# Kernel optimization log

Measured on AMD Instinct MI355X. Metric: run time of the kernel, lower is better.

The kernel has to match this reference:

```python
import jax, jax.numpy as jnp
import numpy as np

B, T = 128, 64          # batch, episode length
OB, AC, L, H = 32, 8, 128, 256  # ob_dim, ac_dim, latent_dim, mlp hidden
N_SUB = 4               # fixed Dopri5 substeps per interval (replaces adaptive PID controller)


def setup_inputs() -> dict:
    key = jax.random.key(0)
    ks = jax.random.split(key, 12)
    g = lambda k, shape, fan: jax.random.normal(k, shape, jnp.float32) / np.sqrt(fan)
    return {
        "ob": jax.random.normal(ks[0], (B, OB), jnp.float32),
        "acs": jax.random.normal(ks[1], (B, T, AC), jnp.float32),
        # strictly increasing timestamps (cumsum of uniform increments)
        "times": jnp.cumsum(jax.random.uniform(ks[2], (B, T), jnp.float32, 0.02, 0.1), axis=1),
        # ob encoder MLP (OB -> H -> L), relu hidden, identity out
        "We0": g(ks[3], (H, OB), OB), "be0": jnp.zeros((H,), jnp.float32),
        "We1": g(ks[4], (L, H), H), "be1": jnp.zeros((L,), jnp.float32),
        # latent dynamics MLP (L -> H -> H -> L)
        "Wd0": g(ks[5], (H, L), L), "bd0": jnp.zeros((H,), jnp.float32),
        "Wd1": g(ks[6], (H, H), H), "bd1": jnp.zeros((H,), jnp.float32),
        "Wd2": g(ks[7], (L, H), H), "bd2": jnp.zeros((L,), jnp.float32),
        # ob decoder MLP (L -> H -> OB)
        "Wo0": g(ks[8], (H, L), L), "bo0": jnp.zeros((H,), jnp.float32),
        "Wo1": g(ks[9], (OB, H), H), "bo1": jnp.zeros((OB,), jnp.float32),
        # GRU cell (input=AC, hidden=L), equinox layout: gates [r, z, n]
        "Wih": g(ks[10], (3 * L, AC), AC), "Whh": g(ks[11], (3 * L, L), L),
        "bih": jnp.zeros((3 * L,), jnp.float32), "bn": jnp.zeros((L,), jnp.float32),
    }


def reference(ob, acs, times, We0, be0, We1, be1, Wd0, bd0, Wd1, bd1, Wd2, bd2,
              Wo0, bo0, Wo1, bo1, Wih, Whh, bih, bn):
    def f(y):  # dynamics MLP on batched latent (B, L) -> (B, L)
        h1 = jax.nn.relu(y @ Wd0.T + bd0)
        h2 = jax.nn.relu(h1 @ Wd1.T + bd1)
        return h2 @ Wd2.T + bd2

    def gru(x, h):  # equinox GRUCell math, batched
        ir, iz, inn = jnp.split(x @ Wih.T + bih, 3, axis=-1)
        hr, hz, hn = jnp.split(h @ Whh.T, 3, axis=-1)
        r = jax.nn.sigmoid(ir + hr)
        z = jax.nn.sigmoid(iz + hz)
        n = jnp.tanh(inn + r * (hn + bn))
        return (1.0 - z) * n + z * h

    def dopri5_step(y, h):  # one Dopri5 (RK45) step, h: (B, 1) per-sample step size
        k1 = f(y)
        k2 = f(y + h * (0.2 * k1))
        k3 = f(y + h * (3/40 * k1 + 9/40 * k2))
        k4 = f(y + h * (44/45 * k1 - 56/15 * k2 + 32/9 * k3))
        k5 = f(y + h * (19372/6561 * k1 - 25360/2187 * k2 + 64448/6561 * k3 - 212/729 * k4))
        k6 = f(y + h * (9017/3168 * k1 - 355/33 * k2 + 46732/5247 * k3 + 49/176 * k4 - 5103/18656 * k5))
        return y + h * (35/384 * k1 + 500/1113 * k3 + 125/192 * k4 - 2187/6784 * k5 + 11/84 * k6)

    def integrate(y, dt):  # integrate latent ODE from 0 to dt with N_SUB fixed Dopri5 steps
        h = (dt / N_SUB)[:, None]
        return jax.lax.fori_loop(0, N_SUB, lambda i, yy: dopri5_step(yy, h), y)

    # encode first observation, consume first action
    latent0 = jax.nn.relu(ob @ We0.T + be0) @ We1.T + be1  # (B, L)
    latent0 = gru(acs[:, 0], latent0)

    dts = jnp.diff(times, axis=1)  # (B, T-1)

    def step(latent, xs):
        ac, dt = xs
        latent = integrate(latent, dt)
        latent = gru(ac, latent)
        return latent, latent

    xs = (jnp.swapaxes(acs[:, 1:], 0, 1), dts.T)  # time-major for scan
    _, lat_seq = jax.lax.scan(step, latent0, xs)  # (T-1, B, L)

    latents = jnp.concatenate([latent0[None], lat_seq], axis=0)  # (T, B, L)
    latents = jnp.swapaxes(latents, 0, 1)  # (B, T, L)

    h1 = jax.nn.relu(latents @ Wo0.T + bo0)
    return h1 @ Wo1.T + bo1  # (B, T, OB)
```

## Files before the change

kernel.cpp:

```cpp
#include <hip/hip_runtime.h>
#include <stdint.h>

#define NBATCH 128
#define NT     64
#define OBD    32
#define ACD    8
#define LDIM   128
#define HDIM   256

typedef _Float16 h2 __attribute__((ext_vector_type(2)));
typedef float    f4 __attribute__((ext_vector_type(4)));

#if defined(__has_builtin)
#  if __has_builtin(__builtin_amdgcn_fdot2)
#    define HAVE_FDOT2 1
#  endif
#endif

__device__ __forceinline__ float dot2f(h2 a, h2 b, float c) {
#ifdef HAVE_FDOT2
  return __builtin_amdgcn_fdot2(a, b, c, false);
#else
  return c + (float)a[0] * (float)b[0] + (float)a[1] * (float)b[1];
#endif
}

__device__ __forceinline__ h2 pkh(float a, float b) {
  h2 r; r[0] = (_Float16)a; r[1] = (_Float16)b; return r;
}

__device__ __forceinline__ h2 bch(float x) { return __builtin_bit_cast(h2, x); }

__device__ __forceinline__ float sigmf(float x) { return 1.0f / (1.0f + expf(-x)); }

#define DOT4(W, I, Q) \
    a0 = dot2f(W[4*(I)+0], bch(Q.x), a0); \
    a1 = dot2f(W[4*(I)+1], bch(Q.y), a1); \
    a2 = dot2f(W[4*(I)+2], bch(Q.z), a2); \
    a3 = dot2f(W[4*(I)+3], bch(Q.w), a3);

__global__ __launch_bounds__(512, 1)
void ode_rnn_kernel(const float* __restrict__ ob,   const float* __restrict__ acs,
                    const float* __restrict__ times,
                    const float* __restrict__ We0,  const float* __restrict__ be0,
                    const float* __restrict__ We1,  const float* __restrict__ be1,
                    const float* __restrict__ Wd0,  const float* __restrict__ bd0,
                    const float* __restrict__ Wd1,  const float* __restrict__ bd1,
                    const float* __restrict__ Wd2,  const float* __restrict__ bd2,
                    const float* __restrict__ Wo0,  const float* __restrict__ bo0,
                    const float* __restrict__ Wo1,  const float* __restrict__ bo1,
                    const float* __restrict__ Wih,  const float* __restrict__ Whh,
                    const float* __restrict__ bih,  const float* __restrict__ bn,
                    float* __restrict__ out)
{
  const int t    = threadIdx.x;
  const int b    = blockIdx.x;
  const int p    = t >> 1;
  const int sub  = t & 1;
  const int r3   = t >> 2;
  const int ksub = t & 3;

  __shared__ __align__(16) float s_lat[LDIM];
  __shared__ __align__(16) float s_k[5][LDIM];
  __shared__ __align__(16) float s_gz[LDIM];
  __shared__ __align__(16) float s_gin[LDIM];
  __shared__ __align__(16) float s_ghn[LDIM];
  __shared__ __align__(16) float s_tmp[HDIM];
  __shared__ __align__(16) float s_obs[OBD];
  __shared__ __align__(16) float s_times[NT];
  __shared__ __align__(16) float s_acs[NT * ACD];
  __shared__ __align__(16) h2    s_in16[LDIM / 2];
  __shared__ __align__(16) h2    s_a16[HDIM / 2];
  __shared__ __align__(16) h2    s_b16[HDIM / 2 + 24];

  h2 w0[32], w1[64], w2[32], q0[32], q1[8];
  {
    const float2* pp = (const float2*)(Wd0 + p * LDIM + sub * 64);
#pragma unroll
    for (int i = 0; i < 32; ++i) { float2 v = pp[i]; w0[i] = pkh(v.x, v.y); }
  }
  {
    const float2* pp = (const float2*)(Wd1 + p * HDIM + sub * 128);
#pragma unroll
    for (int i = 0; i < 64; ++i) { float2 v = pp[i]; w1[i] = pkh(v.x, v.y); }
  }
  {
    const float2* pp = (const float2*)(Wd2 + r3 * HDIM + ksub * 64);
#pragma unroll
    for (int i = 0; i < 32; ++i) { float2 v = pp[i]; w2[i] = pkh(v.x, v.y); }
  }
  {
    const float2* pp = (const float2*)(Wo0 + p * LDIM + sub * 64);
#pragma unroll
    for (int i = 0; i < 32; ++i) { float2 v = pp[i]; q0[i] = pkh(v.x, v.y); }
  }
  {
    const float2* pp = (const float2*)(Wo1 + (t >> 4) * HDIM + (t & 15) * 16);
#pragma unroll
    for (int i = 0; i < 8; ++i) { float2 v = pp[i]; q1[i] = pkh(v.x, v.y); }
  }
  float wi[8];
  if (t < 3 * LDIM) {
#pragma unroll
    for (int j = 0; j < ACD; ++j) wi[j] = Wih[t * ACD + j];
  } else {
#pragma unroll
    for (int j = 0; j < ACD; ++j) wi[j] = 0.0f;
  }

  const float bb0 = bd0[p];
  const float bb1 = bd1[p];
  const float bb2 = bd2[r3];
  const float rb0 = bo0[p];
  const float rb1 = bo1[t >> 4];
  const float gbA = (t < 3 * LDIM) ? bih[t] : 0.0f;
  const float bnr = (t < LDIM) ? bn[t] : 0.0f;

  auto substep = [&](float hs) {
#pragma unroll
    for (int s = 0; s < 6; ++s) {
      float a0, a1, a2, a3, v;
      a0 = a1 = a2 = a3 = 0.0f;
      {
        const f4* src = ((const f4*)s_in16) + sub * 8;
#pragma unroll
        for (int i = 0; i < 8; ++i) { f4 q = src[i]; DOT4(w0, i, q) }
      }
      v = a0 + a1 + a2 + a3;
      v += __shfl_xor(v, 1);
      v = fmaxf(v + bb0, 0.0f);
      { float ov = __shfl_xor(v, 2); if ((t & 3) == 0) s_a16[t >> 2] = pkh(v, ov); }
      __syncthreads();
      a0 = a1 = a2 = a3 = 0.0f;
      {
        const f4* src = ((const f4*)s_a16) + sub * 16;
#pragma unroll
        for (int i = 0; i < 16; ++i) { f4 q = src[i]; DOT4(w1, i, q) }
      }
      v = a0 + a1 + a2 + a3;
      v += __shfl_xor(v, 1);
      v = fmaxf(v + bb1, 0.0f);
      { float ov = __shfl_xor(v, 2);
        if ((t & 3) == 0) s_b16[(t >> 2) + ((t >> 7) << 3)] = pkh(v, ov); }
      __syncthreads();
      a0 = a1 = a2 = a3 = 0.0f;
      {
        const f4* src = ((const f4*)s_b16) + ksub * 10;
#pragma unroll
        for (int i = 0; i < 8; ++i) { f4 q = src[i]; DOT4(w2, i, q) }
      }
      v = a0 + a1 + a2 + a3;
      v += __shfl_xor(v, 1);
      v += __shfl_xor(v, 2);
      float kv = v + bb2;
      if (s < 5 && (t & 3) == 0) s_k[s][r3] = kv;
      float base = s_lat[r3];
      float z;
      if (s == 0)
        z = base + hs * (0.2f * kv);
      else if (s == 1)
        z = base + hs * ((3.0f/40.0f)*s_k[0][r3] + (9.0f/40.0f)*kv);
      else if (s == 2)
        z = base + hs * ((44.0f/45.0f)*s_k[0][r3] - (56.0f/15.0f)*s_k[1][r3]
                       + (32.0f/9.0f)*kv);
      else if (s == 3)
        z = base + hs * ((19372.0f/6561.0f)*s_k[0][r3] - (25360.0f/2187.0f)*s_k[1][r3]
                       + (64448.0f/6561.0f)*s_k[2][r3] - (212.0f/729.0f)*kv);
      else if (s == 4)
        z = base + hs * ((9017.0f/3168.0f)*s_k[0][r3] - (355.0f/33.0f)*s_k[1][r3]
                       + (46732.0f/5247.0f)*s_k[2][r3] + (49.0f/176.0f)*s_k[3][r3]
                       - (5103.0f/18656.0f)*kv);
      else
        z = base + hs * ((35.0f/384.0f)*s_k[0][r3] + (500.0f/1113.0f)*s_k[2][r3]
                       + (125.0f/192.0f)*s_k[3][r3] - (2187.0f/6784.0f)*s_k[4][r3]
                       + (11.0f/84.0f)*kv);
      { float ov = __shfl_xor(z, 4); if ((t & 7) == 0) s_in16[t >> 3] = pkh(z, ov); }
      if (s == 5 && (t & 3) == 0) s_lat[r3] = z;
      __syncthreads();
    }
  };

  auto gru = [&](int ts) {
    __syncthreads();
    float ig = gbA, hg = 0.0f;
    if (t < 3 * LDIM) {
      const float* xa = s_acs + ts * ACD;
#pragma unroll
      for (int j = 0; j < ACD; ++j) ig += wi[j] * xa[j];
      const f4* wh = (const f4*)(Whh + t * LDIM);
      const f4* xl = (const f4*)s_lat;
#pragma unroll
      for (int k2 = 0; k2 < LDIM / 4; ++k2) {
        f4 w = wh[k2], x = xl[k2];
        hg += w.x*x.x + w.y*x.y + w.z*x.z + w.w*x.w;
      }
    }
    if (t >= LDIM && t < 2 * LDIM)          s_gz[t - LDIM] = ig + hg;
    else if (t >= 2 * LDIM && t < 3 * LDIM) { s_gin[t - 2*LDIM] = ig; s_ghn[t - 2*LDIM] = hg; }
    __syncthreads();
    if (t < LDIM) {
      float rg = sigmf(ig + hg);
      float zg = sigmf(s_gz[t]);
      float ng = tanhf(s_gin[t] + rg * (s_ghn[t] + bnr));
      float y  = (1.0f - zg) * ng + zg * s_lat[t];
      s_lat[t] = y;
      float ov = __shfl_xor(y, 1);
      if (!(t & 1)) s_in16[t >> 1] = pkh(y, ov);
    }
  };

  auto decode = [&](int ts) {
    __syncthreads();
    float a0 = 0, a1 = 0, a2 = 0, a3 = 0, v;
    {
      const f4* src = ((const f4*)s_in16) + sub * 8;
#pragma unroll
      for (int i = 0; i < 8; ++i) { f4 q = src[i]; DOT4(q0, i, q) }
    }
    v = a0 + a1 + a2 + a3;
    v += __shfl_xor(v, 1);
    v = fmaxf(v + rb0, 0.0f);
    { float ov = __shfl_xor(v, 2); if ((t & 3) == 0) s_a16[t >> 2] = pkh(v, ov); }
    __syncthreads();
    a0 = a1 = a2 = a3 = 0;
    {
      const f4* src = ((const f4*)s_a16) + (t & 15) * 2;
#pragma unroll
      for (int i = 0; i < 2; ++i) {
        f4 q = src[i];
        a0 = dot2f(q1[4*i+0], bch(q.x), a0);
        a1 = dot2f(q1[4*i+1], bch(q.y), a1);
        a2 = dot2f(q1[4*i+2], bch(q.z), a2);
        a3 = dot2f(q1[4*i+3], bch(q.w), a3);
      }
    }
    v = a0 + a1 + a2 + a3;
    v += __shfl_xor(v, 1);
    v += __shfl_xor(v, 2);
    v += __shfl_xor(v, 4);
    v += __shfl_xor(v, 8);
    if ((t & 15) == 0) out[((size_t)b * NT + ts) * OBD + (t >> 4)] = v + rb1;
    __syncthreads();
  };

  if (t < OBD) s_obs[t] = ob[b * OBD + t];
  if (t < NT)  s_times[t] = times[b * NT + t];
  s_acs[t] = acs[(size_t)b * NT * ACD + t];
  __syncthreads();
  if (t < HDIM) {
    float acc = be0[t];
    const float* wr = We0 + t * OBD;
#pragma unroll
    for (int j = 0; j < OBD; ++j) acc += wr[j] * s_obs[j];
    s_tmp[t] = fmaxf(acc, 0.0f);
  }
  __syncthreads();
  {
    const f4* wr = (const f4*)(We1 + r3 * HDIM + ksub * 64);
    const f4* xs = (const f4*)(s_tmp + ksub * 64);
    float acc = 0.0f;
#pragma unroll
    for (int k = 0; k < 16; ++k) {
      f4 w = wr[k], x = xs[k];
      acc += w.x*x.x + w.y*x.y + w.z*x.z + w.w*x.w;
    }
    acc += __shfl_xor(acc, 1);
    acc += __shfl_xor(acc, 2);
    if ((t & 3) == 0) s_lat[r3] = acc + be1[r3];
  }

  gru(0);
  decode(0);

#pragma unroll 1
  for (int ts = 1; ts < NT; ++ts) {
    float hs = 0.25f * (s_times[ts] - s_times[ts - 1]);
#pragma unroll 1
    for (int su = 0; su < 4; ++su) substep(hs);
    gru(ts);
    decode(ts);
  }
}

extern "C" void kernel_launch(void* const* d_in, const int* in_sizes, int n_in,
                              void* d_out, int out_size, void* d_ws, size_t ws_size,
                              hipStream_t stream) {
  (void)in_sizes; (void)n_in; (void)d_ws; (void)ws_size; (void)out_size;
  const float* ob    = (const float*)d_in[0];
  const float* acs   = (const float*)d_in[1];
  const float* times = (const float*)d_in[2];
  const float* We0   = (const float*)d_in[3];
  const float* be0   = (const float*)d_in[4];
  const float* We1   = (const float*)d_in[5];
  const float* be1   = (const float*)d_in[6];
  const float* Wd0   = (const float*)d_in[7];
  const float* bd0   = (const float*)d_in[8];
  const float* Wd1   = (const float*)d_in[9];
  const float* bd1   = (const float*)d_in[10];
  const float* Wd2   = (const float*)d_in[11];
  const float* bd2   = (const float*)d_in[12];
  const float* Wo0   = (const float*)d_in[13];
  const float* bo0   = (const float*)d_in[14];
  const float* Wo1   = (const float*)d_in[15];
  const float* bo1   = (const float*)d_in[16];
  const float* Wih   = (const float*)d_in[17];
  const float* Whh   = (const float*)d_in[18];
  const float* bih   = (const float*)d_in[19];
  const float* bn    = (const float*)d_in[20];

  ode_rnn_kernel<<<dim3(NBATCH), dim3(512), 0, stream>>>(
      ob, acs, times, We0, be0, We1, be1, Wd0, bd0, Wd1, bd1, Wd2, bd2,
      Wo0, bo0, Wo1, bo1, Wih, Whh, bih, bn, (float*)d_out);
}
```

Before: 2.461 ms.

## Double threads per block to 1024 and split dot products finer

Grows the block from 512 to 1024 threads, so every matvec in the Dopri5 substep, GRU and decoder is split across twice as many lanes. Each lane holds half as many register-resident fp16 weights, and partial sums are combined with extra shuffle stages. Shared-memory activation buffers get padded layouts to reduce bank conflicts. The decoder's first layer now reads Wo0 from global memory each timestep instead of keeping it in registers. Per-lane serial work on the latency-bound recurrence goes down, at the cost of more shuffles, heavier barriers across 16 waves, and extra global weight reads in the decoder.

```diff
diff --git a/kernel.cpp b/kernel.cpp
--- a/kernel.cpp
+++ b/kernel.cpp
@@ -39,7 +39,7 @@
     a2 = dot2f(W[4*(I)+2], bch(Q.z), a2); \
     a3 = dot2f(W[4*(I)+3], bch(Q.w), a3);
 
-__global__ __launch_bounds__(512, 1)
+__global__ __launch_bounds__(1024)
 void ode_rnn_kernel(const float* __restrict__ ob,   const float* __restrict__ acs,
                     const float* __restrict__ times,
                     const float* __restrict__ We0,  const float* __restrict__ be0,
@@ -53,15 +53,20 @@
                     const float* __restrict__ bih,  const float* __restrict__ bn,
                     float* __restrict__ out)
 {
-  const int t    = threadIdx.x;
-  const int b    = blockIdx.x;
-  const int p    = t >> 1;
-  const int sub  = t & 1;
-  const int r3   = t >> 2;
-  const int ksub = t & 3;
+  const int t  = threadIdx.x;
+  const int b  = blockIdx.x;
+  const int p  = t >> 2;
+  const int qs = t & 3;
+  const int r  = t >> 3;
+  const int es = t & 7;
+  const int o  = t >> 5;
+  const int s5 = t & 31;
+  const int gr = t >> 1;
+  const int kh = t & 1;
 
   __shared__ __align__(16) float s_lat[LDIM];
   __shared__ __align__(16) float s_k[5][LDIM];
+  __shared__ __align__(16) float s_gr[LDIM];
   __shared__ __align__(16) float s_gz[LDIM];
   __shared__ __align__(16) float s_gin[LDIM];
   __shared__ __align__(16) float s_ghn[LDIM];
@@ -69,51 +74,50 @@
   __shared__ __align__(16) float s_obs[OBD];
   __shared__ __align__(16) float s_times[NT];
   __shared__ __align__(16) float s_acs[NT * ACD];
-  __shared__ __align__(16) h2    s_in16[LDIM / 2];
-  __shared__ __align__(16) h2    s_a16[HDIM / 2];
-  __shared__ __align__(16) h2    s_b16[HDIM / 2 + 24];
-
-  h2 w0[32], w1[64], w2[32], q0[32], q1[8];
-  {
-    const float2* pp = (const float2*)(Wd0 + p * LDIM + sub * 64);
-#pragma unroll
-    for (int i = 0; i < 32; ++i) { float2 v = pp[i]; w0[i] = pkh(v.x, v.y); }
-  }
-  {
-    const float2* pp = (const float2*)(Wd1 + p * HDIM + sub * 128);
-#pragma unroll
-    for (int i = 0; i < 64; ++i) { float2 v = pp[i]; w1[i] = pkh(v.x, v.y); }
-  }
-  {
-    const float2* pp = (const float2*)(Wd2 + r3 * HDIM + ksub * 64);
-#pragma unroll
-    for (int i = 0; i < 32; ++i) { float2 v = pp[i]; w2[i] = pkh(v.x, v.y); }
-  }
-  {
-    const float2* pp = (const float2*)(Wo0 + p * LDIM + sub * 64);
-#pragma unroll
-    for (int i = 0; i < 32; ++i) { float2 v = pp[i]; q0[i] = pkh(v.x, v.y); }
-  }
-  {
-    const float2* pp = (const float2*)(Wo1 + (t >> 4) * HDIM + (t & 15) * 16);
-#pragma unroll
-    for (int i = 0; i < 8; ++i) { float2 v = pp[i]; q1[i] = pkh(v.x, v.y); }
-  }
-  float wi[8];
-  if (t < 3 * LDIM) {
-#pragma unroll
-    for (int j = 0; j < ACD; ++j) wi[j] = Wih[t * ACD + j];
+  __shared__ __align__(16) h2    s_in16[80];
+  __shared__ __align__(16) h2    s_a16[144];
+  __shared__ __align__(16) h2    s_b16[160];
+
+#define W16(i) ((i) + (((i) >> 4) << 2))
+#define WA(i)  ((i) + (((i) >> 5) << 2))
+#define WB(i)  ((i) + (((i) >> 4) << 2))
+
+  h2 w0[16], w1[32], w2[16], q1[4];
+  {
+    const float2* pp = (const float2*)(Wd0 + p * LDIM + qs * 32);
+#pragma unroll
+    for (int i = 0; i < 16; ++i) { float2 v = pp[i]; w0[i] = pkh(v.x, v.y); }
+  }
+  {
+    const float2* pp = (const float2*)(Wd1 + p * HDIM + qs * 64);
+#pragma unroll
+    for (int i = 0; i < 32; ++i) { float2 v = pp[i]; w1[i] = pkh(v.x, v.y); }
+  }
+  {
+    const float2* pp = (const float2*)(Wd2 + r * HDIM + es * 32);
+#pragma unroll
+    for (int i = 0; i < 16; ++i) { float2 v = pp[i]; w2[i] = pkh(v.x, v.y); }
+  }
+  {
+    const float2* pp = (const float2*)(Wo1 + o * HDIM + s5 * 8);
+#pragma unroll
+    for (int i = 0; i < 4; ++i) { float2 v = pp[i]; q1[i] = pkh(v.x, v.y); }
+  }
+  float wi[4];
+  if (gr < 3 * LDIM) {
+#pragma unroll
+    for (int j = 0; j < 4; ++j) wi[j] = Wih[gr * ACD + kh * 4 + j];
   } else {
 #pragma unroll
-    for (int j = 0; j < ACD; ++j) wi[j] = 0.0f;
+    for (int j = 0; j < 4; ++j) wi[j] = 0.0f;
   }
 
   const float bb0 = bd0[p];
   const float bb1 = bd1[p];
-  const float bb2 = bd2[r3];
+  const float bb2 = bd2[r];
   const float rb0 = bo0[p];
-  const float rb1 = bo1[t >> 4];
-  const float gbA = (t < 3 * LDIM) ? bih[t] : 0.0f;
+  const float rb1 = bo1[o];
+  const float gA  = (gr < 3 * LDIM) ? bih[gr] : 0.0f;
   const float bnr = (t < LDIM) ? bn[t] : 0.0f;
 
   auto substep = [&](float hs) {
@@ -122,130 +126,138 @@
       float a0, a1, a2, a3, v;
       a0 = a1 = a2 = a3 = 0.0f;
       {
-        const f4* src = ((const f4*)s_in16) + sub * 8;
-#pragma unroll
-        for (int i = 0; i < 8; ++i) { f4 q = src[i]; DOT4(w0, i, q) }
-      }
-      v = a0 + a1 + a2 + a3;
+        const f4* src = ((const f4*)s_in16) + qs * 5;
+#pragma unroll
+        for (int i = 0; i < 4; ++i) { f4 q = src[i]; DOT4(w0, i, q) }
+      }
+      v = (a0 + a1) + (a2 + a3);
       v += __shfl_xor(v, 1);
+      v += __shfl_xor(v, 2);
       v = fmaxf(v + bb0, 0.0f);
-      { float ov = __shfl_xor(v, 2); if ((t & 3) == 0) s_a16[t >> 2] = pkh(v, ov); }
+      { float ov = __shfl_xor(v, 4); if ((t & 7) == 0) s_a16[WA(t >> 3)] = pkh(v, ov); }
       __syncthreads();
       a0 = a1 = a2 = a3 = 0.0f;
       {
-        const f4* src = ((const f4*)s_a16) + sub * 16;
-#pragma unroll
-        for (int i = 0; i < 16; ++i) { f4 q = src[i]; DOT4(w1, i, q) }
-      }
-      v = a0 + a1 + a2 + a3;
+        const f4* src = ((const f4*)s_a16) + qs * 9;
+#pragma unroll
+        for (int i = 0; i < 8; ++i) { f4 q = src[i]; DOT4(w1, i, q) }
+      }
+      v = (a0 + a1) + (a2 + a3);
       v += __shfl_xor(v, 1);
+      v += __shfl_xor(v, 2);
       v = fmaxf(v + bb1, 0.0f);
-      { float ov = __shfl_xor(v, 2);
-        if ((t & 3) == 0) s_b16[(t >> 2) + ((t >> 7) << 3)] = pkh(v, ov); }
+      { float ov = __shfl_xor(v, 4); if ((t & 7) == 0) s_b16[WB(t >> 3)] = pkh(v, ov); }
       __syncthreads();
       a0 = a1 = a2 = a3 = 0.0f;
       {
-        const f4* src = ((const f4*)s_b16) + ksub * 10;
-#pragma unroll
-        for (int i = 0; i < 8; ++i) { f4 q = src[i]; DOT4(w2, i, q) }
-      }
-      v = a0 + a1 + a2 + a3;
+        const f4* src = ((const f4*)s_b16) + es * 5;
+#pragma unroll
+        for (int i = 0; i < 4; ++i) { f4 q = src[i]; DOT4(w2, i, q) }
+      }
+      v = (a0 + a1) + (a2 + a3);
       v += __shfl_xor(v, 1);
       v += __shfl_xor(v, 2);
+      v += __shfl_xor(v, 4);
       float kv = v + bb2;
-      if (s < 5 && (t & 3) == 0) s_k[s][r3] = kv;
-      float base = s_lat[r3];
+      if (s < 5 && es == 0) s_k[s][r] = kv;
+      float base = s_lat[r];
       float z;
       if (s == 0)
         z = base + hs * (0.2f * kv);
       else if (s == 1)
-        z = base + hs * ((3.0f/40.0f)*s_k[0][r3] + (9.0f/40.0f)*kv);
+        z = base + hs * ((3.0f/40.0f)*s_k[0][r] + (9.0f/40.0f)*kv);
       else if (s == 2)
-        z = base + hs * ((44.0f/45.0f)*s_k[0][r3] - (56.0f/15.0f)*s_k[1][r3]
+        z = base + hs * ((44.0f/45.0f)*s_k[0][r] - (56.0f/15.0f)*s_k[1][r]
                        + (32.0f/9.0f)*kv);
       else if (s == 3)
-        z = base + hs * ((19372.0f/6561.0f)*s_k[0][r3] - (25360.0f/2187.0f)*s_k[1][r3]
-                       + (64448.0f/6561.0f)*s_k[2][r3] - (212.0f/729.0f)*kv);
+        z = base + hs * ((19372.0f/6561.0f)*s_k[0][r] - (25360.0f/2187.0f)*s_k[1][r]
+                       + (64448.0f/6561.0f)*s_k[2][r] - (212.0f/729.0f)*kv);
       else if (s == 4)
-        z = base + hs * ((9017.0f/3168.0f)*s_k[0][r3] - (355.0f/33.0f)*s_k[1][r3]
-                       + (46732.0f/5247.0f)*s_k[2][r3] + (49.0f/176.0f)*s_k[3][r3]
+        z = base + hs * ((9017.0f/3168.0f)*s_k[0][r] - (355.0f/33.0f)*s_k[1][r]
+                       + (46732.0f/5247.0f)*s_k[2][r] + (49.0f/176.0f)*s_k[3][r]
                        - (5103.0f/18656.0f)*kv);
       else
-        z = base + hs * ((35.0f/384.0f)*s_k[0][r3] + (500.0f/1113.0f)*s_k[2][r3]
-                       + (125.0f/192.0f)*s_k[3][r3] - (2187.0f/6784.0f)*s_k[4][r3]
+        z = base + hs * ((35.0f/384.0f)*s_k[0][r] + (500.0f/1113.0f)*s_k[2][r]
+                       + (125.0f/192.0f)*s_k[3][r] - (2187.0f/6784.0f)*s_k[4][r]
                        + (11.0f/84.0f)*kv);
-      { float ov = __shfl_xor(z, 4); if ((t & 7) == 0) s_in16[t >> 3] = pkh(z, ov); }
-      if (s == 5 && (t & 3) == 0) s_lat[r3] = z;
+      { float ov = __shfl_xor(z, 8); if ((t & 15) == 0) s_in16[W16(t >> 4)] = pkh(z, ov); }
+      if (s == 5 && es == 0) s_lat[r] = z;
       __syncthreads();
     }
   };
 
   auto gru = [&](int ts) {
     __syncthreads();
-    float ig = gbA, hg = 0.0f;
-    if (t < 3 * LDIM) {
-      const float* xa = s_acs + ts * ACD;
-#pragma unroll
-      for (int j = 0; j < ACD; ++j) ig += wi[j] * xa[j];
-      const f4* wh = (const f4*)(Whh + t * LDIM);
-      const f4* xl = (const f4*)s_lat;
-#pragma unroll
-      for (int k2 = 0; k2 < LDIM / 4; ++k2) {
+    float vi = 0.0f, vh = 0.0f;
+    if (gr < 3 * LDIM) {
+      const float* xa = s_acs + ts * ACD + kh * 4;
+#pragma unroll
+      for (int j = 0; j < 4; ++j) vi += wi[j] * xa[j];
+      const f4* wh = (const f4*)(Whh + gr * LDIM + kh * 64);
+      const f4* xl = ((const f4*)s_lat) + kh * 16;
+#pragma unroll
+      for (int k2 = 0; k2 < 16; ++k2) {
         f4 w = wh[k2], x = xl[k2];
-        hg += w.x*x.x + w.y*x.y + w.z*x.z + w.w*x.w;
-      }
-    }
-    if (t >= LDIM && t < 2 * LDIM)          s_gz[t - LDIM] = ig + hg;
-    else if (t >= 2 * LDIM && t < 3 * LDIM) { s_gin[t - 2*LDIM] = ig; s_ghn[t - 2*LDIM] = hg; }
+        vh += w.x*x.x + w.y*x.y + w.z*x.z + w.w*x.w;
+      }
+    }
+    vi += __shfl_xor(vi, 1);
+    vh += __shfl_xor(vh, 1);
+    if (gr < 3 * LDIM && kh == 0) {
+      if (gr < LDIM)           s_gr[gr] = vi + gA + vh;
+      else if (gr < 2 * LDIM)  s_gz[gr - LDIM] = vi + gA + vh;
+      else                   { s_gin[gr - 2*LDIM] = vi + gA; s_ghn[gr - 2*LDIM] = vh; }
+    }
     __syncthreads();
     if (t < LDIM) {
-      float rg = sigmf(ig + hg);
+      float rg = sigmf(s_gr[t]);
       float zg = sigmf(s_gz[t]);
       float ng = tanhf(s_gin[t] + rg * (s_ghn[t] + bnr));
       float y  = (1.0f - zg) * ng + zg * s_lat[t];
       s_lat[t] = y;
       float ov = __shfl_xor(y, 1);
-      if (!(t & 1)) s_in16[t >> 1] = pkh(y, ov);
+      if (!(t & 1)) s_in16[W16(t >> 1)] = pkh(y, ov);
     }
   };
 
   auto decode = [&](int ts) {
     __syncthreads();
-    float a0 = 0, a1 = 0, a2 = 0, a3 = 0, v;
+    float acc = 0.0f;
     {
-      const f4* src = ((const f4*)s_in16) + sub * 8;
-#pragma unroll
-      for (int i = 0; i < 8; ++i) { f4 q = src[i]; DOT4(q0, i, q) }
-    }
-    v = a0 + a1 + a2 + a3;
-    v += __shfl_xor(v, 1);
-    v = fmaxf(v + rb0, 0.0f);
-    { float ov = __shfl_xor(v, 2); if ((t & 3) == 0) s_a16[t >> 2] = pkh(v, ov); }
-    __syncthreads();
-    a0 = a1 = a2 = a3 = 0;
+      const f4* wr = (const f4*)(Wo0 + p * LDIM + qs * 32);
+      const f4* xl = ((const f4*)s_lat) + qs * 8;
+#pragma unroll
+      for (int k2 = 0; k2 < 8; ++k2) {
+        f4 w = wr[k2], x = xl[k2];
+        acc += w.x*x.x + w.y*x.y + w.z*x.z + w.w*x.w;
+      }
+    }
+    acc += __shfl_xor(acc, 1);
+    acc += __shfl_xor(acc, 2);
+    acc = fmaxf(acc + rb0, 0.0f);
+    { float ov = __shfl_xor(acc, 4); if ((t & 7) == 0) s_a16[WA(t >> 3)] = pkh(acc, ov); }
+    __syncthreads();
+    float a0 = 0, a1 = 0, a2 = 0, a3 = 0;
     {
-      const f4* src = ((const f4*)s_a16) + (t & 15) * 2;
-#pragma unroll
-      for (int i = 0; i < 2; ++i) {
-        f4 q = src[i];
-        a0 = dot2f(q1[4*i+0], bch(q.x), a0);
-        a1 = dot2f(q1[4*i+1], bch(q.y), a1);
-        a2 = dot2f(q1[4*i+2], bch(q.z), a2);
-        a3 = dot2f(q1[4*i+3], bch(q.w), a3);
-      }
-    }
-    v = a0 + a1 + a2 + a3;
+      const f4 q = *(((const f4*)s_a16) + s5 + (s5 >> 3));
+      a0 = dot2f(q1[0], bch(q.x), a0);
+      a1 = dot2f(q1[1], bch(q.y), a1);
+      a2 = dot2f(q1[2], bch(q.z), a2);
+      a3 = dot2f(q1[3], bch(q.w), a3);
+    }
+    float v = (a0 + a1) + (a2 + a3);
     v += __shfl_xor(v, 1);
     v += __shfl_xor(v, 2);
     v += __shfl_xor(v, 4);
     v += __shfl_xor(v, 8);
-    if ((t & 15) == 0) out[((size_t)b * NT + ts) * OBD + (t >> 4)] = v + rb1;
+    v += __shfl_xor(v, 16);
+    if (s5 == 0) out[((size_t)b * NT + ts) * OBD + o] = v + rb1;
     __syncthreads();
   };
 
   if (t < OBD) s_obs[t] = ob[b * OBD + t];
   if (t < NT)  s_times[t] = times[b * NT + t];
-  s_acs[t] = acs[(size_t)b * NT * ACD + t];
+  if (t < NT * ACD) s_acs[t] = acs[(size_t)b * NT * ACD + t];
   __syncthreads();
   if (t < HDIM) {
     float acc = be0[t];
@@ -256,17 +268,18 @@
   }
   __syncthreads();
   {
-    const f4* wr = (const f4*)(We1 + r3 * HDIM + ksub * 64);
-    const f4* xs = (const f4*)(s_tmp + ksub * 64);
+    const f4* wr = (const f4*)(We1 + r * HDIM + es * 32);
+    const f4* xs = ((const f4*)s_tmp) + es * 8;
     float acc = 0.0f;
 #pragma unroll
-    for (int k = 0; k < 16; ++k) {
+    for (int k = 0; k < 8; ++k) {
       f4 w = wr[k], x = xs[k];
       acc += w.x*x.x + w.y*x.y + w.z*x.z + w.w*x.w;
     }
     acc += __shfl_xor(acc, 1);
     acc += __shfl_xor(acc, 2);
-    if ((t & 3) == 0) s_lat[r3] = acc + be1[r3];
+    acc += __shfl_xor(acc, 4);
+    if (es == 0) s_lat[r] = acc + be1[r];
   }
 
   gru(0);
@@ -308,7 +321,7 @@
   const float* bih   = (const float*)d_in[19];
   const float* bn    = (const float*)d_in[20];
 
-  ode_rnn_kernel<<<dim3(NBATCH), dim3(512), 0, stream>>>(
+  ode_rnn_kernel<<<dim3(NBATCH), dim3(1024), 0, stream>>>(
       ob, acs, times, We0, be0, We1, be1, Wd0, bd0, Wd1, bd1, Wd2, bd2,
       Wo0, bo0, Wo1, bo1, Wih, Whh, bih, bn, (float*)d_out);
 }
```

New measurement: 2.866 ms. 16.5% more time.

## Move Wd1 weights to padded LDS and drop decoder/GRU register-cached weights

Applied to the files above, without the earlier changes.

Stores the fp16-packed Wd1 dynamics weights in dynamic shared memory with a padded per-thread stride instead of registers. Decoder and GRU input weights are now read from global fp32 each use rather than kept in registers. The aim is to relieve VGPR pressure (possible spills) at 512 threads per block. In exchange, each substep's second layer reads weights from LDS, and the kernel needs about 133KB of dynamic LDS.

```diff
diff --git a/kernel.cpp b/kernel.cpp
--- a/kernel.cpp
+++ b/kernel.cpp
@@ -7,6 +7,9 @@
 #define ACD    8
 #define LDIM   128
 #define HDIM   256
+
+#define W1_STRIDE 65
+#define W1_BYTES  (512 * W1_STRIDE * 4)
 
 typedef _Float16 h2 __attribute__((ext_vector_type(2)));
 typedef float    f4 __attribute__((ext_vector_type(4)));
@@ -39,7 +42,11 @@
     a2 = dot2f(W[4*(I)+2], bch(Q.z), a2); \
     a3 = dot2f(W[4*(I)+3], bch(Q.w), a3);
 
-__global__ __launch_bounds__(512, 1)
+#define PB(i) ((i) + (((i) >> 5) << 2))
+
+extern __shared__ h2 w1s[];
+
+__global__ __launch_bounds__(512)
 void ode_rnn_kernel(const float* __restrict__ ob,   const float* __restrict__ acs,
                     const float* __restrict__ times,
                     const float* __restrict__ We0,  const float* __restrict__ be0,
@@ -57,7 +64,7 @@
   const int b    = blockIdx.x;
   const int p    = t >> 1;
   const int sub  = t & 1;
-  const int r3   = t >> 2;
+  const int r    = t >> 2;
   const int ksub = t & 3;
 
   __shared__ __align__(16) float s_lat[LDIM];
@@ -71,49 +78,35 @@
   __shared__ __align__(16) float s_acs[NT * ACD];
   __shared__ __align__(16) h2    s_in16[LDIM / 2];
   __shared__ __align__(16) h2    s_a16[HDIM / 2];
-  __shared__ __align__(16) h2    s_b16[HDIM / 2 + 24];
-
-  h2 w0[32], w1[64], w2[32], q0[32], q1[8];
+  __shared__ __align__(16) h2    s_b16[HDIM / 2 + 12];
+
+  h2 w0[32], w2[32];
   {
     const float2* pp = (const float2*)(Wd0 + p * LDIM + sub * 64);
 #pragma unroll
     for (int i = 0; i < 32; ++i) { float2 v = pp[i]; w0[i] = pkh(v.x, v.y); }
   }
   {
-    const float2* pp = (const float2*)(Wd1 + p * HDIM + sub * 128);
-#pragma unroll
-    for (int i = 0; i < 64; ++i) { float2 v = pp[i]; w1[i] = pkh(v.x, v.y); }
+    const float2* pp = (const float2*)(Wd2 + r * HDIM + ksub * 64);
+#pragma unroll
+    for (int i = 0; i < 32; ++i) { float2 v = pp[i]; w2[i] = pkh(v.x, v.y); }
   }
   {
-    const float2* pp = (const float2*)(Wd2 + r3 * HDIM + ksub * 64);
-#pragma unroll
-    for (int i = 0; i < 32; ++i) { float2 v = pp[i]; w2[i] = pkh(v.x, v.y); }
-  }
-  {
-    const float2* pp = (const float2*)(Wo0 + p * LDIM + sub * 64);
-#pragma unroll
-    for (int i = 0; i < 32; ++i) { float2 v = pp[i]; q0[i] = pkh(v.x, v.y); }
-  }
-  {
-    const float2* pp = (const float2*)(Wo1 + (t >> 4) * HDIM + (t & 15) * 16);
-#pragma unroll
-    for (int i = 0; i < 8; ++i) { float2 v = pp[i]; q1[i] = pkh(v.x, v.y); }
-  }
-  float wi[8];
-  if (t < 3 * LDIM) {
-#pragma unroll
-    for (int j = 0; j < ACD; ++j) wi[j] = Wih[t * ACD + j];
-  } else {
-#pragma unroll
-    for (int j = 0; j < ACD; ++j) wi[j] = 0.0f;
+    const f4* src = (const f4*)(Wd1 + p * HDIM + sub * 128);
+    const int base = t * W1_STRIDE;
+#pragma unroll
+    for (int i = 0; i < 32; ++i) {
+      f4 q = src[i];
+      w1s[base + 2*i]     = pkh(q.x, q.y);
+      w1s[base + 2*i + 1] = pkh(q.z, q.w);
+    }
   }
 
   const float bb0 = bd0[p];
   const float bb1 = bd1[p];
-  const float bb2 = bd2[r3];
+  const float bb2 = bd2[r];
   const float rb0 = bo0[p];
-  const float rb1 = bo1[t >> 4];
-  const float gbA = (t < 3 * LDIM) ? bih[t] : 0.0f;
+  const float gA  = (t < 3 * LDIM) ? bih[t] : 0.0f;
   const float bnr = (t < LDIM) ? bn[t] : 0.0f;
 
   auto substep = [&](float hs) {
@@ -126,80 +119,88 @@
 #pragma unroll
         for (int i = 0; i < 8; ++i) { f4 q = src[i]; DOT4(w0, i, q) }
       }
-      v = a0 + a1 + a2 + a3;
+      v = (a0 + a1) + (a2 + a3);
       v += __shfl_xor(v, 1);
       v = fmaxf(v + bb0, 0.0f);
       { float ov = __shfl_xor(v, 2); if ((t & 3) == 0) s_a16[t >> 2] = pkh(v, ov); }
       __syncthreads();
       a0 = a1 = a2 = a3 = 0.0f;
       {
-        const f4* src = ((const f4*)s_a16) + sub * 16;
-#pragma unroll
-        for (int i = 0; i < 16; ++i) { f4 q = src[i]; DOT4(w1, i, q) }
-      }
-      v = a0 + a1 + a2 + a3;
+        const f4* act  = ((const f4*)s_a16) + sub * 16;
+        const h2* wrow = w1s + t * W1_STRIDE;
+#pragma unroll
+        for (int i = 0; i < 16; ++i) {
+          f4 q = act[i];
+          a0 = dot2f(wrow[4*i+0], bch(q.x), a0);
+          a1 = dot2f(wrow[4*i+1], bch(q.y), a1);
+          a2 = dot2f(wrow[4*i+2], bch(q.z), a2);
+          a3 = dot2f(wrow[4*i+3], bch(q.w), a3);
+        }
+      }
+      v = (a0 + a1) + (a2 + a3);
       v += __shfl_xor(v, 1);
       v = fmaxf(v + bb1, 0.0f);
-      { float ov = __shfl_xor(v, 2);
-        if ((t & 3) == 0) s_b16[(t >> 2) + ((t >> 7) << 3)] = pkh(v, ov); }
+      { float ov = __shfl_xor(v, 2); if ((t & 3) == 0) s_b16[PB(t >> 2)] = pkh(v, ov); }
       __syncthreads();
       a0 = a1 = a2 = a3 = 0.0f;
       {
-        const f4* src = ((const f4*)s_b16) + ksub * 10;
+        const f4* src = ((const f4*)s_b16) + ksub * 9;
 #pragma unroll
         for (int i = 0; i < 8; ++i) { f4 q = src[i]; DOT4(w2, i, q) }
       }
-      v = a0 + a1 + a2 + a3;
+      v = (a0 + a1) + (a2 + a3);
       v += __shfl_xor(v, 1);
       v += __shfl_xor(v, 2);
       float kv = v + bb2;
-      if (s < 5 && (t & 3) == 0) s_k[s][r3] = kv;
-      float base = s_lat[r3];
+      if (s < 5 && ksub == 0) s_k[s][r] = kv;
+      float base = s_lat[r];
       float z;
       if (s == 0)
         z = base + hs * (0.2f * kv);
       else if (s == 1)
-        z = base + hs * ((3.0f/40.0f)*s_k[0][r3] + (9.0f/40.0f)*kv);
+        z = base + hs * ((3.0f/40.0f)*s_k[0][r] + (9.0f/40.0f)*kv);
       else if (s == 2)
-        z = base + hs * ((44.0f/45.0f)*s_k[0][r3] - (56.0f/15.0f)*s_k[1][r3]
+        z = base + hs * ((44.0f/45.0f)*s_k[0][r] - (56.0f/15.0f)*s_k[1][r]
                        + (32.0f/9.0f)*kv);
       else if (s == 3)
-        z = base + hs * ((19372.0f/6561.0f)*s_k[0][r3] - (25360.0f/2187.0f)*s_k[1][r3]
-                       + (64448.0f/6561.0f)*s_k[2][r3] - (212.0f/729.0f)*kv);
+        z = base + hs * ((19372.0f/6561.0f)*s_k[0][r] - (25360.0f/2187.0f)*s_k[1][r]
+                       + (64448.0f/6561.0f)*s_k[2][r] - (212.0f/729.0f)*kv);
       else if (s == 4)
-        z = base + hs * ((9017.0f/3168.0f)*s_k[0][r3] - (355.0f/33.0f)*s_k[1][r3]
-                       + (46732.0f/5247.0f)*s_k[2][r3] + (49.0f/176.0f)*s_k[3][r3]
+        z = base + hs * ((9017.0f/3168.0f)*s_k[0][r] - (355.0f/33.0f)*s_k[1][r]
+                       + (46732.0f/5247.0f)*s_k[2][r] + (49.0f/176.0f)*s_k[3][r]
                        - (5103.0f/18656.0f)*kv);
       else
-        z = base + hs * ((35.0f/384.0f)*s_k[0][r3] + (500.0f/1113.0f)*s_k[2][r3]
-                       + (125.0f/192.0f)*s_k[3][r3] - (2187.0f/6784.0f)*s_k[4][r3]
+        z = base + hs * ((35.0f/384.0f)*s_k[0][r] + (500.0f/1113.0f)*s_k[2][r]
+                       + (125.0f/192.0f)*s_k[3][r] - (2187.0f/6784.0f)*s_k[4][r]
                        + (11.0f/84.0f)*kv);
       { float ov = __shfl_xor(z, 4); if ((t & 7) == 0) s_in16[t >> 3] = pkh(z, ov); }
-      if (s == 5 && (t & 3) == 0) s_lat[r3] = z;
+      if (s == 5 && ksub == 0) s_lat[r] = z;
       __syncthreads();
     }
   };
 
   auto gru = [&](int ts) {
     __syncthreads();
-    float ig = gbA, hg = 0.0f;
+    float vi = gA, vh = 0.0f;
     if (t < 3 * LDIM) {
       const float* xa = s_acs + ts * ACD;
-#pragma unroll
-      for (int j = 0; j < ACD; ++j) ig += wi[j] * xa[j];
+      const f4* wiv = (const f4*)(Wih + t * ACD);
+      f4 wa = wiv[0], wb = wiv[1];
+      vi += wa.x*xa[0] + wa.y*xa[1] + wa.z*xa[2] + wa.w*xa[3]
+          + wb.x*xa[4] + wb.y*xa[5] + wb.z*xa[6] + wb.w*xa[7];
       const f4* wh = (const f4*)(Whh + t * LDIM);
       const f4* xl = (const f4*)s_lat;
 #pragma unroll
       for (int k2 = 0; k2 < LDIM / 4; ++k2) {
         f4 w = wh[k2], x = xl[k2];
-        hg += w.x*x.x + w.y*x.y + w.z*x.z + w.w*x.w;
-      }
-    }
-    if (t >= LDIM && t < 2 * LDIM)          s_gz[t - LDIM] = ig + hg;
-    else if (t >= 2 * LDIM && t < 3 * LDIM) { s_gin[t - 2*LDIM] = ig; s_ghn[t - 2*LDIM] = hg; }
+        vh += w.x*x.x + w.y*x.y + w.z*x.z + w.w*x.w;
+      }
+    }
+    if (t >= LDIM && t < 2 * LDIM)          s_gz[t - LDIM] = vi + vh;
+    else if (t >= 2 * LDIM && t < 3 * LDIM) { s_gin[t - 2*LDIM] = vi; s_ghn[t - 2*LDIM] = vh; }
     __syncthreads();
     if (t < LDIM) {
-      float rg = sigmf(ig + hg);
+      float rg = sigmf(vi + vh);
       float zg = sigmf(s_gz[t]);
       float ng = tanhf(s_gin[t] + rg * (s_ghn[t] + bnr));
       float y  = (1.0f - zg) * ng + zg * s_lat[t];
@@ -211,35 +212,39 @@
 
   auto decode = [&](int ts) {
     __syncthreads();
-    float a0 = 0, a1 = 0, a2 = 0, a3 = 0, v;
+    float acc = 0.0f;
     {
-      const f4* src = ((const f4*)s_in16) + sub * 8;
-#pragma unroll
-      for (int i = 0; i < 8; ++i) { f4 q = src[i]; DOT4(q0, i, q) }
-    }
-    v = a0 + a1 + a2 + a3;
-    v += __shfl_xor(v, 1);
-    v = fmaxf(v + rb0, 0.0f);
-    { float ov = __shfl_xor(v, 2); if ((t & 3) == 0) s_a16[t >> 2] = pkh(v, ov); }
-    __syncthreads();
-    a0 = a1 = a2 = a3 = 0;
+      const f4* wr = (const f4*)(Wo0 + p * LDIM + sub * 64);
+      const f4* xl = ((const f4*)s_lat) + sub * 16;
+#pragma unroll
+      for (int k2 = 0; k2 < 16; ++k2) {
+        f4 w = wr[k2], x = xl[k2];
+        acc += w.x*x.x + w.y*x.y + w.z*x.z + w.w*x.w;
+      }
+    }
+    acc += __shfl_xor(acc, 1);
+    acc = fmaxf(acc + rb0, 0.0f);
+    { float ov = __shfl_xor(acc, 2); if ((t & 3) == 0) s_a16[t >> 2] = pkh(acc, ov); }
+    __syncthreads();
+    const int o  = t >> 4;
+    const int sl = t & 15;
+    float v2 = 0.0f;
     {
-      const f4* src = ((const f4*)s_a16) + (t & 15) * 2;
-#pragma unroll
-      for (int i = 0; i < 2; ++i) {
-        f4 q = src[i];
-        a0 = dot2f(q1[4*i+0], bch(q.x), a0);
-        a1 = dot2f(q1[4*i+1], bch(q.y), a1);
-        a2 = dot2f(q1[4*i+2], bch(q.z), a2);
-        a3 = dot2f(q1[4*i+3], bch(q.w), a3);
-      }
-    }
-    v = a0 + a1 + a2 + a3;
-    v += __shfl_xor(v, 1);
-    v += __shfl_xor(v, 2);
-    v += __shfl_xor(v, 4);
-    v += __shfl_xor(v, 8);
-    if ((t & 15) == 0) out[((size_t)b * NT + ts) * OBD + (t >> 4)] = v + rb1;
+      const f4* wr = (const f4*)(Wo1 + o * HDIM + sl * 16);
+      const h2* xs = s_a16 + sl * 8;
+#pragma unroll
+      for (int i = 0; i < 4; ++i) {
+        f4 w = wr[i];
+        h2 xa = xs[2*i], xb = xs[2*i+1];
+        v2 += w.x*(float)xa[0] + w.y*(float)xa[1]
+            + w.z*(float)xb[0] + w.w*(float)xb[1];
+      }
+    }
+    v2 += __shfl_xor(v2, 1);
+    v2 += __shfl_xor(v2, 2);
+    v2 += __shfl_xor(v2, 4);
+    v2 += __shfl_xor(v2, 8);
+    if (sl == 0) out[((size_t)b * NT + ts) * OBD + o] = v2 + bo1[o];
     __syncthreads();
   };
 
@@ -256,8 +261,8 @@
   }
   __syncthreads();
   {
-    const f4* wr = (const f4*)(We1 + r3 * HDIM + ksub * 64);
-    const f4* xs = (const f4*)(s_tmp + ksub * 64);
+    const f4* wr = (const f4*)(We1 + r * HDIM + ksub * 64);
+    const f4* xs = ((const f4*)s_tmp) + ksub * 16;
     float acc = 0.0f;
 #pragma unroll
     for (int k = 0; k < 16; ++k) {
@@ -266,7 +271,7 @@
     }
     acc += __shfl_xor(acc, 1);
     acc += __shfl_xor(acc, 2);
-    if ((t & 3) == 0) s_lat[r3] = acc + be1[r3];
+    if (ksub == 0) s_lat[r] = acc + be1[r];
   }
 
   gru(0);
@@ -308,7 +313,9 @@
   const float* bih   = (const float*)d_in[19];
   const float* bn    = (const float*)d_in[20];
 
-  ode_rnn_kernel<<<dim3(NBATCH), dim3(512), 0, stream>>>(
+  hipFuncSetAttribute((const void*)ode_rnn_kernel,
+                      hipFuncAttributeMaxDynamicSharedMemorySize, W1_BYTES);
+  ode_rnn_kernel<<<dim3(NBATCH), dim3(512), W1_BYTES, stream>>>(
       ob, acs, times, We0, be0, We1, be1, Wd0, bd0, Wd1, bd1, Wd2, bd2,
       Wo0, bo0, Wo1, bo1, Wih, Whh, bih, bn, (float*)d_out);
 }
```

Result: slower. 3.172 ms (+28.9%).
